# Optimization experiments

Hardware: AMD Instinct MI355X
Metric: run time of the kernel (lower is better)

Reference implementation:

```python
import jax, jax.numpy as jnp
import numpy as np

B, S, H, K = 4, 4096, 2048, 4
EPS = 1e-6

def rmsnorm(x, w, eps=EPS):
    xf = x.astype(jnp.float32)
    var = jnp.mean(xf * xf, axis=-1, keepdims=True)
    return (w * (xf * jax.lax.rsqrt(var + eps)).astype(x.dtype))

def setup_inputs() -> dict:
    key = jax.random.key(0)
    k1, k2, k3 = jax.random.split(key, 3)
    hidden_states = jax.random.normal(k1, (B, S, H), dtype=jnp.float32)
    norm_weight = jnp.ones((H,), dtype=jnp.float32)
    conv_weight = jax.random.normal(k2, (H, 1, K), dtype=jnp.float32) * 0.1
    conv_bias = jax.random.normal(k3, (H,), dtype=jnp.float32) * 0.1
    return {"hidden_states": hidden_states, "norm_weight": norm_weight,
            "conv_weight": conv_weight, "conv_bias": conv_bias}

def reference(hidden_states, norm_weight, conv_weight, conv_bias):
    # RMSNorm over hidden dim
    x = rmsnorm(hidden_states, norm_weight)          # [B, S, H]
    x = jnp.transpose(x, (0, 2, 1))                  # [B, H, S] (NCH)
    # Depthwise causal conv1d: left-pad K-1 so output length == S
    y = jax.lax.conv_general_dilated(
        x, conv_weight,                              # [H, 1, K] (OIH), groups=H
        window_strides=(1,),
        padding=[(K - 1, 0)],
        dimension_numbers=("NCH", "OIH", "NCH"),
        feature_group_count=H,
    )                                                # [B, H, S]
    y = y + conv_bias[None, :, None]
    return jnp.transpose(y, (0, 2, 1))               # [B, S, H]
```

## Files before the change

### kernel.cpp

```cpp
#include <hip/hip_runtime.h>


#define BQ 4
#define SQ 4096
#define HQ 2048
#define KQ 4
#define TROWS 32
#define RB 4
#define NGRP (TROWS / RB + 1)
#define NTHREADS 512
#define NWAVES (NTHREADS / 64)

typedef float f32x4 __attribute__((ext_vector_type(4)));

__global__ __launch_bounds__(NTHREADS, 4) void ttt_conv_kernel(
    const float* __restrict__ x,
    const float* __restrict__ gamma,
    const float* __restrict__ cwp,
    const float* __restrict__ cbp,
    float* __restrict__ out)
{
    __shared__ float part[2][RB][NWAVES];

    const int tid  = threadIdx.x;
    const int lane = tid & 63;
    const int wid  = tid >> 6;

    const int tilesPerB = SQ / TROWS;
    const int b  = blockIdx.x / tilesPerB;
    const int s0 = (blockIdx.x % tilesPerB) * TROWS;
    const int h4 = tid * 4;

    const float4 g4    = *reinterpret_cast<const float4*>(gamma + h4);
    const float4 bias4 = *reinterpret_cast<const float4*>(cbp + h4);
    const float4 r0 = *reinterpret_cast<const float4*>(cwp + (size_t)(h4 + 0) * KQ);
    const float4 r1 = *reinterpret_cast<const float4*>(cwp + (size_t)(h4 + 1) * KQ);
    const float4 r2 = *reinterpret_cast<const float4*>(cwp + (size_t)(h4 + 2) * KQ);
    const float4 r3 = *reinterpret_cast<const float4*>(cwp + (size_t)(h4 + 3) * KQ);
    const float4 c0 = make_float4(r0.x, r1.x, r2.x, r3.x);
    const float4 c1 = make_float4(r0.y, r1.y, r2.y, r3.y);
    const float4 c2 = make_float4(r0.z, r1.z, r2.z, r3.z);
    const float4 c3 = make_float4(r0.w, r1.w, r2.w, r3.w);

    const float* xb = x   + (size_t)b * SQ * HQ + h4;
    float*       ob = out + (size_t)b * SQ * HQ + h4;

    const float4 f4z = make_float4(0.f, 0.f, 0.f, 0.f);
    float4 wm3 = f4z, wm2 = f4z, wm1 = f4z;

    float4 buf[RB];
    {
        const int base = s0 - RB;
        #pragma unroll
        for (int r = 0; r < RB; ++r) {
            const int s = base + r;
            buf[r] = (s >= 0) ? *reinterpret_cast<const float4*>(xb + (size_t)s * HQ)
                              : f4z;
        }
    }

    for (int g = 0; g < NGRP; ++g) {
        const int base = s0 - RB + g * RB;

        float4 cur[RB];
        #pragma unroll
        for (int r = 0; r < RB; ++r) cur[r] = buf[r];

        float p[RB];
        #pragma unroll
        for (int r = 0; r < RB; ++r)
            p[r] = cur[r].x * cur[r].x + cur[r].y * cur[r].y
                 + cur[r].z * cur[r].z + cur[r].w * cur[r].w;

        if (g + 1 < NGRP) {
            const int nb = base + RB;
            #pragma unroll
            for (int r = 0; r < RB; ++r) {
                const int s = nb + r;
                buf[r] = (s >= 0) ? *reinterpret_cast<const float4*>(xb + (size_t)s * HQ)
                                  : f4z;
            }
        }

        #pragma unroll
        for (int off = 32; off >= 1; off >>= 1) {
            #pragma unroll
            for (int r = 0; r < RB; ++r)
                p[r] += __shfl_xor(p[r], off, 64);
        }
        if (lane == 0) {
            #pragma unroll
            for (int r = 0; r < RB; ++r) part[g & 1][r][wid] = p[r];
        }
        __syncthreads();

        float tot[RB];
        #pragma unroll
        for (int r = 0; r < RB; ++r) {
            const float4 pa = *reinterpret_cast<const float4*>(&part[g & 1][r][0]);
            const float4 pb = *reinterpret_cast<const float4*>(&part[g & 1][r][4]);
            tot[r] = (pa.x + pa.y + pa.z + pa.w) + (pb.x + pb.y + pb.z + pb.w);
        }

        #pragma unroll
        for (int r = 0; r < RB; ++r) {
            const float scale = rsqrtf(tot[r] * (1.0f / HQ) + 1e-6f);
            float4 xn;
            xn.x = cur[r].x * scale * g4.x;
            xn.y = cur[r].y * scale * g4.y;
            xn.z = cur[r].z * scale * g4.z;
            xn.w = cur[r].w * scale * g4.w;

            if (g > 0) {
                f32x4 o;
                o.x = bias4.x + c0.x * wm3.x + c1.x * wm2.x + c2.x * wm1.x + c3.x * xn.x;
                o.y = bias4.y + c0.y * wm3.y + c1.y * wm2.y + c2.y * wm1.y + c3.y * xn.y;
                o.z = bias4.z + c0.z * wm3.z + c1.z * wm2.z + c2.z * wm1.z + c3.z * xn.z;
                o.w = bias4.w + c0.w * wm3.w + c1.w * wm2.w + c2.w * wm1.w + c3.w * xn.w;
                const int s = base + r;
                __builtin_nontemporal_store(
                    o, reinterpret_cast<f32x4*>(ob + (size_t)s * HQ));
            }
            wm3 = wm2; wm2 = wm1; wm1 = xn;
        }
    }
}

extern "C" void kernel_launch(void* const* d_in, const int* in_sizes, int n_in,
                              void* d_out, int out_size, void* d_ws, size_t ws_size,
                              hipStream_t stream) {
    const float* x  = (const float*)d_in[0];
    const float* nw = (const float*)d_in[1];
    const float* cw = (const float*)d_in[2];
    const float* cb = (const float*)d_in[3];
    float* o = (float*)d_out;

    const int grid = BQ * (SQ / TROWS);
    ttt_conv_kernel<<<grid, NTHREADS, 0, stream>>>(x, nw, cw, cb, o);
}
```

Measured before the change: 241.8 us.

## Split RMSNorm scale computation into separate pre-pass kernel

Computes per-row RMS scales in a separate kernel written to workspace, then the conv kernel reads scales instead of doing block-wide reductions with shared memory and __syncthreads. Gamma is folded into the conv weights. This removes the per-group synchronization and the redundant halo-row reduction, at the cost of reading the input twice from memory (possibly partly served by last-level cache).

```diff
diff --git a/kernel.cpp b/kernel.cpp
--- a/kernel.cpp
+++ b/kernel.cpp
@@ -5,27 +5,48 @@
 #define SQ 4096
 #define HQ 2048
 #define KQ 4
+#define ROWS (BQ * SQ)
 #define TROWS 32
-#define RB 4
-#define NGRP (TROWS / RB + 1)
-#define NTHREADS 512
-#define NWAVES (NTHREADS / 64)
+#define NT2 512
 
 typedef float f32x4 __attribute__((ext_vector_type(4)));
 
-__global__ __launch_bounds__(NTHREADS, 4) void ttt_conv_kernel(
+__global__ __launch_bounds__(256) void ttt_scale_kernel(
+    const float* __restrict__ x,
+    float* __restrict__ sc)
+{
+    const int lane = threadIdx.x & 63;
+    const int row  = blockIdx.x * 4 + (threadIdx.x >> 6);
+
+    const float* xr = x + (size_t)row * HQ + lane * 4;
+
+    float4 v[8];
+    #pragma unroll
+    for (int i = 0; i < 8; ++i)
+        v[i] = *reinterpret_cast<const float4*>(xr + i * 256);
+
+    float p = 0.f;
+    #pragma unroll
+    for (int i = 0; i < 8; ++i)
+        p += v[i].x * v[i].x + v[i].y * v[i].y + v[i].z * v[i].z + v[i].w * v[i].w;
+
+    #pragma unroll
+    for (int off = 32; off >= 1; off >>= 1)
+        p += __shfl_xor(p, off, 64);
+
+    if (lane == 0)
+        sc[row] = rsqrtf(p * (1.0f / HQ) + 1e-6f);
+}
+
+__global__ __launch_bounds__(NT2) void ttt_conv_kernel(
     const float* __restrict__ x,
     const float* __restrict__ gamma,
     const float* __restrict__ cwp,
     const float* __restrict__ cbp,
+    const float* __restrict__ sc,
     float* __restrict__ out)
 {
-    __shared__ float part[2][RB][NWAVES];
-
-    const int tid  = threadIdx.x;
-    const int lane = tid & 63;
-    const int wid  = tid >> 6;
-
+    const int tid = threadIdx.x;
     const int tilesPerB = SQ / TROWS;
     const int b  = blockIdx.x / tilesPerB;
     const int s0 = (blockIdx.x % tilesPerB) * TROWS;
@@ -37,90 +58,69 @@
     const float4 r1 = *reinterpret_cast<const float4*>(cwp + (size_t)(h4 + 1) * KQ);
     const float4 r2 = *reinterpret_cast<const float4*>(cwp + (size_t)(h4 + 2) * KQ);
     const float4 r3 = *reinterpret_cast<const float4*>(cwp + (size_t)(h4 + 3) * KQ);
-    const float4 c0 = make_float4(r0.x, r1.x, r2.x, r3.x);
-    const float4 c1 = make_float4(r0.y, r1.y, r2.y, r3.y);
-    const float4 c2 = make_float4(r0.z, r1.z, r2.z, r3.z);
-    const float4 c3 = make_float4(r0.w, r1.w, r2.w, r3.w);
+    float4 c0 = make_float4(r0.x * g4.x, r1.x * g4.y, r2.x * g4.z, r3.x * g4.w);
+    float4 c1 = make_float4(r0.y * g4.x, r1.y * g4.y, r2.y * g4.z, r3.y * g4.w);
+    float4 c2 = make_float4(r0.z * g4.x, r1.z * g4.y, r2.z * g4.z, r3.z * g4.w);
+    float4 c3 = make_float4(r0.w * g4.x, r1.w * g4.y, r2.w * g4.z, r3.w * g4.w);
 
-    const float* xb = x   + (size_t)b * SQ * HQ + h4;
-    float*       ob = out + (size_t)b * SQ * HQ + h4;
+    const float* xb  = x   + (size_t)b * SQ * HQ + h4;
+    float*       ob  = out + (size_t)b * SQ * HQ + h4;
+    const float* scb = sc  + (size_t)b * SQ;
 
     const float4 f4z = make_float4(0.f, 0.f, 0.f, 0.f);
     float4 wm3 = f4z, wm2 = f4z, wm1 = f4z;
 
-    float4 buf[RB];
-    {
-        const int base = s0 - RB;
-        #pragma unroll
-        for (int r = 0; r < RB; ++r) {
-            const int s = base + r;
-            buf[r] = (s >= 0) ? *reinterpret_cast<const float4*>(xb + (size_t)s * HQ)
-                              : f4z;
+    #pragma unroll
+    for (int k = 0; k < 3; ++k) {
+        const int s = s0 - 3 + k;
+        float4 w = f4z;
+        if (s >= 0) {
+            const float4 xv = *reinterpret_cast<const float4*>(xb + (size_t)s * HQ);
+            const float sv = scb[s];
+            w.x = xv.x * sv; w.y = xv.y * sv; w.z = xv.z * sv; w.w = xv.w * sv;
         }
+        if (k == 0) wm3 = w; else if (k == 1) wm2 = w; else wm1 = w;
     }
 
-    for (int g = 0; g < NGRP; ++g) {
-        const int base = s0 - RB + g * RB;
+    float4 buf[4];
+    float4 scn;
+    #pragma unroll
+    for (int r = 0; r < 4; ++r)
+        buf[r] = *reinterpret_cast<const float4*>(xb + (size_t)(s0 + r) * HQ);
+    scn = *reinterpret_cast<const float4*>(scb + s0);
 
-        float4 cur[RB];
+    for (int g = 0; g < TROWS / 4; ++g) {
+        const int base = s0 + g * 4;
+
+        float4 cur[4];
         #pragma unroll
-        for (int r = 0; r < RB; ++r) cur[r] = buf[r];
+        for (int r = 0; r < 4; ++r) cur[r] = buf[r];
+        const float4 scv = scn;
 
-        float p[RB];
-        #pragma unroll
-        for (int r = 0; r < RB; ++r)
-            p[r] = cur[r].x * cur[r].x + cur[r].y * cur[r].y
-                 + cur[r].z * cur[r].z + cur[r].w * cur[r].w;
-
-        if (g + 1 < NGRP) {
-            const int nb = base + RB;
+        if (g + 1 < TROWS / 4) {
+            const int nb = base + 4;
             #pragma unroll
-            for (int r = 0; r < RB; ++r) {
-                const int s = nb + r;
-                buf[r] = (s >= 0) ? *reinterpret_cast<const float4*>(xb + (size_t)s * HQ)
-                                  : f4z;
-            }
+            for (int r = 0; r < 4; ++r)
+                buf[r] = *reinterpret_cast<const float4*>(xb + (size_t)(nb + r) * HQ);
+            scn = *reinterpret_cast<const float4*>(scb + nb);
         }
 
+        const float svs[4] = { scv.x, scv.y, scv.z, scv.w };
         #pragma unroll
-        for (int off = 32; off >= 1; off >>= 1) {
-            #pragma unroll
-            for (int r = 0; r < RB; ++r)
-                p[r] += __shfl_xor(p[r], off, 64);
-        }
-        if (lane == 0) {
-            #pragma unroll
-            for (int r = 0; r < RB; ++r) part[g & 1][r][wid] = p[r];
-        }
-        __syncthreads();
+        for (int r = 0; r < 4; ++r) {
+            const float sv = svs[r];
+            float4 xn;
+            xn.x = cur[r].x * sv; xn.y = cur[r].y * sv;
+            xn.z = cur[r].z * sv; xn.w = cur[r].w * sv;
 
-        float tot[RB];
-        #pragma unroll
-        for (int r = 0; r < RB; ++r) {
-            const float4 pa = *reinterpret_cast<const float4*>(&part[g & 1][r][0]);
-            const float4 pb = *reinterpret_cast<const float4*>(&part[g & 1][r][4]);
-            tot[r] = (pa.x + pa.y + pa.z + pa.w) + (pb.x + pb.y + pb.z + pb.w);
-        }
+            f32x4 o;
+            o.x = bias4.x + c0.x * wm3.x + c1.x * wm2.x + c2.x * wm1.x + c3.x * xn.x;
+            o.y = bias4.y + c0.y * wm3.y + c1.y * wm2.y + c2.y * wm1.y + c3.y * xn.y;
+            o.z = bias4.z + c0.z * wm3.z + c1.z * wm2.z + c2.z * wm1.z + c3.z * xn.z;
+            o.w = bias4.w + c0.w * wm3.w + c1.w * wm2.w + c2.w * wm1.w + c3.w * xn.w;
+            __builtin_nontemporal_store(
+                o, reinterpret_cast<f32x4*>(ob + (size_t)(base + r) * HQ));
 
-        #pragma unroll
-        for (int r = 0; r < RB; ++r) {
-            const float scale = rsqrtf(tot[r] * (1.0f / HQ) + 1e-6f);
-            float4 xn;
-            xn.x = cur[r].x * scale * g4.x;
-            xn.y = cur[r].y * scale * g4.y;
-            xn.z = cur[r].z * scale * g4.z;
-            xn.w = cur[r].w * scale * g4.w;
-
-            if (g > 0) {
-                f32x4 o;
-                o.x = bias4.x + c0.x * wm3.x + c1.x * wm2.x + c2.x * wm1.x + c3.x * xn.x;
-                o.y = bias4.y + c0.y * wm3.y + c1.y * wm2.y + c2.y * wm1.y + c3.y * xn.y;
-                o.z = bias4.z + c0.z * wm3.z + c1.z * wm2.z + c2.z * wm1.z + c3.z * xn.z;
-                o.w = bias4.w + c0.w * wm3.w + c1.w * wm2.w + c2.w * wm1.w + c3.w * xn.w;
-                const int s = base + r;
-                __builtin_nontemporal_store(
-                    o, reinterpret_cast<f32x4*>(ob + (size_t)s * HQ));
-            }
             wm3 = wm2; wm2 = wm1; wm1 = xn;
         }
     }
@@ -133,8 +133,9 @@
     const float* nw = (const float*)d_in[1];
     const float* cw = (const float*)d_in[2];
     const float* cb = (const float*)d_in[3];
-    float* o = (float*)d_out;
+    float* o  = (float*)d_out;
+    float* sc = (float*)d_ws;
 
-    const int grid = BQ * (SQ / TROWS);
-    ttt_conv_kernel<<<grid, NTHREADS, 0, stream>>>(x, nw, cw, cb, o);
+    ttt_scale_kernel<<<ROWS / 4, 256, 0, stream>>>(x, sc);
+    ttt_conv_kernel<<<BQ * (SQ / TROWS), NT2, 0, stream>>>(x, nw, cw, cb, sc, o);
 }
```

Measured after the change: 252.9 us. +4.6%, slower.
